# Performance work log

Measured on AMD Instinct MI355X. Metric: run time of the kernel, lower is better.

Reference implementation:

```python
import jax, jax.numpy as jnp
import numpy as np

P, U, D, B = 10000, 8000, 64, 4096
NG, ND, NU, NPU = 320000, 320000, 400000, 400000
TEMP = 0.2
L_GEO, L_DI, L_MV = 2, 2, 2


def _spmm(rows, cols, vals, x, n_out):
    # sparse [n_out, n_in] @ x [n_in, D] as gather + segment-sum (COO spmm)
    return jax.ops.segment_sum(vals[:, None] * x[cols], rows, num_segments=n_out)


def _l2norm(x):
    return x / jnp.maximum(jnp.linalg.norm(x, axis=1, keepdims=True), 1e-12)


def _infonce(e1, e2):
    pos = jnp.exp(jnp.sum(e1 * e2, axis=1) / TEMP)
    neg = jnp.sum(jnp.exp(e1 @ e2.T / TEMP), axis=1)
    return jnp.mean(-jnp.log(pos / (neg + 1e-8) + 1e-8))


def setup_inputs() -> dict:
    key = jax.random.key(0)
    ks = jax.random.split(key, 32)
    f = jax.random.normal
    ri = jax.random.randint
    return {
        "poi_emb": f(ks[0], (P + 1, D)) * 0.1,
        "user_emb": f(ks[1], (U, D)) * 0.1,
        "w_gate_geo": f(ks[2], (D, D)) * 0.1,
        "b_gate_geo": f(ks[3], (1, D)) * 0.1,
        "w_gate_seq": f(ks[4], (D, D)) * 0.1,
        "b_gate_seq": f(ks[5], (1, D)) * 0.1,
        "w_gate_col": f(ks[6], (D, D)) * 0.1,
        "b_gate_col": f(ks[7], (1, D)) * 0.1,
        "fusion_w": f(ks[8], (7 * D, D)) * 0.05,
        "fusion_b": f(ks[9], (D,)) * 0.05,
        "geo_vals": jax.random.uniform(ks[10], (NG,)) / 32.0,
        "src_vals": jax.random.uniform(ks[11], (ND,)) / 32.0,
        "tar_vals": jax.random.uniform(ks[12], (ND,)) / 32.0,
        "up_vals": jax.random.uniform(ks[13], (NU,)) / 50.0,
        "pu_vals": jax.random.uniform(ks[14], (NPU,)) / 50.0,
        "geo_rows": ri(ks[15], (NG,), 0, P),
        "geo_cols": ri(ks[16], (NG,), 0, P),
        "src_rows": ri(ks[17], (ND,), 0, P),
        "src_cols": ri(ks[18], (ND,), 0, P),
        "tar_rows": ri(ks[19], (ND,), 0, P),
        "tar_cols": ri(ks[20], (ND,), 0, P),
        "up_rows": ri(ks[21], (NU,), 0, U),
        "up_cols": ri(ks[22], (NU,), 0, P),
        "pu_rows": ri(ks[23], (NPU,), 0, P),
        "pu_cols": ri(ks[24], (NPU,), 0, U),
        "user_idx": ri(ks[25], (B,), 0, U),
    }


def reference(poi_emb, user_emb, w_gate_geo, b_gate_geo, w_gate_seq, b_gate_seq,
              w_gate_col, b_gate_col, fusion_w, fusion_b,
              geo_vals, src_vals, tar_vals, up_vals, pu_vals,
              geo_rows, geo_cols, src_rows, src_cols, tar_rows, tar_cols,
              up_rows, up_cols, pu_rows, pu_cols, user_idx):
    pe = poi_emb[:-1]  # [P, D], drop padding row
    gate = lambda w, b: pe * jax.nn.sigmoid(pe @ w + b)
    geo_g = gate(w_gate_geo, b_gate_geo)
    seq_g = gate(w_gate_seq, b_gate_seq)
    col_g = gate(w_gate_col, b_gate_col)

    # GeoConvNetwork: residual spmm layers, mean over all layer outputs
    x = geo_g
    acc = [x]
    for _ in range(L_GEO):
        x = _spmm(geo_rows, geo_cols, geo_vals, x, P) + acc[-1]
        acc.append(x)
    geo_pois = sum(acc) / (L_GEO + 1)

    # DirectedHyperConvNetwork: HG_src @ (HG_tar @ x), residual, mean
    x = seq_g
    acc = [x]
    for _ in range(L_DI):
        m = _spmm(tar_rows, tar_cols, tar_vals, x, P)
        x = _spmm(src_rows, src_cols, src_vals, m, P) + acc[-1]
        acc.append(x)
    seq_pois = sum(acc) / (L_DI + 1)

    ng = _l2norm(geo_pois)
    ns = _l2norm(seq_pois)
    loss_cl = 0.5 * (_infonce(ng, ns) + _infonce(ns, ng))

    # MultiSemanticHyperConvNetwork: layer input is always the init embeddings
    acc = [col_g]
    for _ in range(L_MV):
        m_geo = _spmm(up_rows, up_cols, up_vals, ng, U)
        m_seq = _spmm(up_rows, up_cols, up_vals, ns, U)
        m_poi = _spmm(up_rows, up_cols, up_vals, col_g, U)
        msg = jnp.concatenate([m_geo, m_seq, m_poi,
                               m_geo * m_seq, m_geo * m_poi, m_seq * m_poi,
                               m_geo * m_seq * m_poi], axis=1)  # [U, 7D]
        msg_emb = msg @ fusion_w + fusion_b
        hg_users = msg_emb + user_emb + msg_emb * user_emb
        x = _spmm(pu_rows, pu_cols, pu_vals, hg_users, P) + acc[-1]
        acc.append(x)
    hg_pois = sum(acc) / (L_MV + 1)

    fusion_pois = _l2norm(hg_pois) + ng + ns
    users_struct = _spmm(up_rows, up_cols, up_vals, fusion_pois, U)
    batch_users = _l2norm(users_struct[user_idx])
    return batch_users, fusion_pois, loss_cl
```

## Files before the change

kernel.cpp:

```cpp
#include <hip/hip_runtime.h>

#define PN 10000
#define UN 8000
#define BN 4096
#define NGE 320000
#define NDE 320000
#define NUE 400000
#define NPUE 400000
#define SCALE_BF 2.6857914f
#define E0 320000
#define E1 640000
#define E2 960000
#define E3 1360000
#define E4 1760000

#define SCHUNK 4096
#define NC_A 79
#define NC_B 158
#define NC_C 237
#define NC_D 335
#define NCT 433
#define RPB_P 79
#define RPB_U 63
#define MAGIC_P 53093u
#define MAGIC_U 66577u

#define HW_P 32
#define HW_U 40
#define PT_GEO 0
#define PT_TAR 320000
#define PT_SRC 640000
#define PT_UP  960000
#define PT_PU  1280000

#define NSTR 79

typedef __attribute__((ext_vector_type(8))) short short8;
typedef __attribute__((ext_vector_type(4))) float f32x4;
typedef unsigned short u16;
typedef unsigned int u32;

__device__ __forceinline__ u16 f2bf(float x) {
    u32 u = __float_as_uint(x);
    return (u16)((u + 0x7FFFu + ((u >> 16) & 1u)) >> 16);
}

__global__ void gates3_kernel(const float* __restrict__ poi,
                              const float* __restrict__ w0, const float* __restrict__ b0,
                              const float* __restrict__ w1, const float* __restrict__ b1,
                              const float* __restrict__ w2, const float* __restrict__ b2,
                              float* __restrict__ o0, float* __restrict__ o1, float* __restrict__ o2) {
    __shared__ float W[3][64][64];
    __shared__ float Bv[3][64];
    __shared__ float pe[4][64];
    int tid = threadIdx.x;
    for (int t = tid; t < 4096; t += 256) {
        int k = t >> 6, j = t & 63;
        W[0][k][j] = w0[t]; W[1][k][j] = w1[t]; W[2][k][j] = w2[t];
    }
    if (tid < 64) { Bv[0][tid] = b0[tid]; Bv[1][tid] = b1[tid]; Bv[2][tid] = b2[tid]; }
    int r0 = blockIdx.x * 4;
    {
        int r = tid >> 6, k = tid & 63;
        pe[r][k] = poi[(r0 + r) * 64 + k];
    }
    __syncthreads();
    int r = tid >> 6, j = tid & 63;
    float pj = pe[r][j];
    int o = (r0 + r) * 64 + j;
    float out[3];
#pragma unroll
    for (int g = 0; g < 3; g++) {
        float acc = Bv[g][j];
#pragma unroll
        for (int k = 0; k < 64; k++) acc += pe[r][k] * W[g][k][j];
        out[g] = pj * (1.0f / (1.0f + __expf(-acc)));
    }
    o0[o] = out[0]; o1[o] = out[1]; o2[o] = out[2];
}

__global__ __launch_bounds__(256) void hist_lds_kernel(
        const int* __restrict__ r0, const int* __restrict__ r1,
        const int* __restrict__ r2, const int* __restrict__ r3,
        const int* __restrict__ r4, int* __restrict__ part) {
    __shared__ int h[PN];
    int b = blockIdx.x, tid = threadIdx.x;
    const int* rows; int n; int l; int* pp;
    if (b < 32)       { rows = r0; n = PN; l = b;       pp = part + PT_GEO + l * PN; }
    else if (b < 64)  { rows = r1; n = PN; l = b - 32;  pp = part + PT_TAR + l * PN; }
    else if (b < 96)  { rows = r2; n = PN; l = b - 64;  pp = part + PT_SRC + l * PN; }
    else if (b < 136) { rows = r3; n = UN; l = b - 96;  pp = part + PT_UP  + l * UN; }
    else              { rows = r4; n = PN; l = b - 136; pp = part + PT_PU  + l * PN; }
    for (int i = tid; i < n; i += 256) h[i] = 0;
    __syncthreads();
    int base4 = l * 2500;
    for (int j = tid; j < 2500; j += 256) {
        int4 rv = ((const int4*)rows)[base4 + j];
        atomicAdd(&h[rv.x], 1);
        atomicAdd(&h[rv.y], 1);
        atomicAdd(&h[rv.z], 1);
        atomicAdd(&h[rv.w], 1);
    }
    __syncthreads();
    for (int i = tid; i < n; i += 256) pp[i] = h[i];
}

__global__ __launch_bounds__(256) void sum_partials_kernel(const int* __restrict__ part,
                                                           int* __restrict__ t0, int* __restrict__ t1,
                                                           int* __restrict__ t2, int* __restrict__ t3,
                                                           int* __restrict__ t4) {
    int t = blockIdx.x * 256 + threadIdx.x;
    const int* pp; int* tot; int n; int W; int i;
    if (t < 10000)      { pp = part + PT_GEO; tot = t0; n = PN; W = HW_P; i = t; }
    else if (t < 20000) { pp = part + PT_TAR; tot = t1; n = PN; W = HW_P; i = t - 10000; }
    else if (t < 30000) { pp = part + PT_SRC; tot = t2; n = PN; W = HW_P; i = t - 20000; }
    else if (t < 38000) { pp = part + PT_UP;  tot = t3; n = UN; W = HW_U; i = t - 30000; }
    else if (t < 48000) { pp = part + PT_PU;  tot = t4; n = PN; W = HW_U; i = t - 38000; }
    else return;
    int s = 0;
    for (int w = 0; w < W; w++) s += pp[w * n + i];
    tot[i] = s;
}

__global__ __launch_bounds__(1024) void scan_lds_kernel(
        const int* __restrict__ t0, const int* __restrict__ t1,
        const int* __restrict__ t2, const int* __restrict__ t3,
        const int* __restrict__ t4,
        int* p0, int* p1, int* p2, int* p3, int* p4) {
    __shared__ int h[PN];
    __shared__ int ps[1024];
    const int* tot; int* rp; int n; int nnz;
    switch (blockIdx.x) {
        case 0: tot = t0; rp = p0; n = PN; nnz = NGE;  break;
        case 1: tot = t1; rp = p1; n = PN; nnz = NDE;  break;
        case 2: tot = t2; rp = p2; n = PN; nnz = NDE;  break;
        case 3: tot = t3; rp = p3; n = UN; nnz = NUE;  break;
        default: tot = t4; rp = p4; n = PN; nnz = NPUE; break;
    }
    int tid = threadIdx.x;
    for (int i = tid; i < n; i += 1024) h[i] = tot[i];
    __syncthreads();
    int chunk = (n + 1023) >> 10;
    int base = tid * chunk;
    int s = 0;
#pragma unroll
    for (int k = 0; k < 10; k++) {
        int i = base + k;
        if (k < chunk && i < n) s += h[i];
    }
    ps[tid] = s;
    __syncthreads();
    for (int off = 1; off < 1024; off <<= 1) {
        int v = (tid >= off) ? ps[tid - off] : 0;
        __syncthreads();
        ps[tid] += v;
        __syncthreads();
    }
    int pre = (tid > 0) ? ps[tid - 1] : 0;
#pragma unroll
    for (int k = 0; k < 10; k++) {
        int i = base + k;
        if (k < chunk && i < n) {
            int c = h[i];
            rp[i] = pre;
            pre += c;
        }
    }
    if (tid == 0) rp[n] = nnz;
}

__global__ void init_bcur_kernel(const int* __restrict__ rp0, const int* __restrict__ rp1,
                                 const int* __restrict__ rp2, const int* __restrict__ rp3,
                                 const int* __restrict__ rp4, int* __restrict__ bcur) {
    int t = blockIdx.x * 256 + threadIdx.x;
    if (t >= 640) return;
    int m = t >> 7, b = t & 127;
    const int* rp; int n; int rpb;
    switch (m) {
        case 0: rp = rp0; n = PN; rpb = RPB_P; break;
        case 1: rp = rp1; n = PN; rpb = RPB_P; break;
        case 2: rp = rp2; n = PN; rpb = RPB_P; break;
        case 3: rp = rp3; n = UN; rpb = RPB_U; break;
        default: rp = rp4; n = PN; rpb = RPB_P; break;
    }
    int r = b * rpb; if (r > n) r = n;
    bcur[t] = rp[r];
}

__global__ __launch_bounds__(256) void scatter_p1_kernel(
        const int* __restrict__ r0, const int* __restrict__ k0, const float* __restrict__ v0, int2* __restrict__ t0,
        const int* __restrict__ r1, const int* __restrict__ k1, const float* __restrict__ v1, int2* __restrict__ t1,
        const int* __restrict__ r2, const int* __restrict__ k2, const float* __restrict__ v2, int2* __restrict__ t2,
        const int* __restrict__ r3, const int* __restrict__ k3, const float* __restrict__ v3, int2* __restrict__ t3,
        const int* __restrict__ r4, const int* __restrict__ k4, const float* __restrict__ v4, int2* __restrict__ t4,
        int* __restrict__ bcur) {
    __shared__ int cnt[128];
    __shared__ int2 stage[128 * 64];
    int tid = threadIdx.x;
    int c = blockIdx.x;
    const int* rr; const int* cc; const float* vv; int2* tt; int n; int lc; int m; u32 magic;
    if (c < NC_A)      { rr = r0; cc = k0; vv = v0; tt = t0; n = NGE;  lc = c;        m = 0; magic = MAGIC_P; }
    else if (c < NC_B) { rr = r1; cc = k1; vv = v1; tt = t1; n = NDE;  lc = c - NC_A; m = 1; magic = MAGIC_P; }
    else if (c < NC_C) { rr = r2; cc = k2; vv = v2; tt = t2; n = NDE;  lc = c - NC_B; m = 2; magic = MAGIC_P; }
    else if (c < NC_D) { rr = r3; cc = k3; vv = v3; tt = t3; n = NUE;  lc = c - NC_C; m = 3; magic = MAGIC_U; }
    else               { rr = r4; cc = k4; vv = v4; tt = t4; n = NPUE; lc = c - NC_D; m = 4; magic = MAGIC_P; }
    if (tid < 128) cnt[tid] = 0;
    __syncthreads();
    int* gc = bcur + (m << 7);
    int base4 = lc * (SCHUNK / 4);
#pragma unroll
    for (int s = 0; s < 4; s++) {
        int e4i = base4 + s * 256 + tid;
        if (e4i * 4 < n) {
            int4   rv = ((const int4*)rr)[e4i];
            int4   cv = ((const int4*)cc)[e4i];
            float4 wv = ((const float4*)vv)[e4i];
            int rws[4] = {rv.x, rv.y, rv.z, rv.w};
            int cls[4] = {cv.x, cv.y, cv.z, cv.w};
            float vls[4] = {wv.x, wv.y, wv.z, wv.w};
#pragma unroll
            for (int q = 0; q < 4; q++) {
                int row = rws[q];
                int b = (int)(((u32)row * magic) >> 22);
                int2 ent = make_int2((row << 16) | cls[q], __float_as_int(vls[q]));
                int sl = atomicAdd(&cnt[b], 1);
                if (sl < 64) stage[(b << 6) + sl] = ent;
                else { int p = atomicAdd(&gc[b], 1); tt[p] = ent; }
            }
        }
    }
    __syncthreads();
    if (tid < 128) {
        int cc2 = cnt[tid]; if (cc2 > 64) cc2 = 64;
        if (cc2 > 0) {
            int p = atomicAdd(&gc[tid], cc2);
            for (int k = 0; k < cc2; k++) tt[p + k] = stage[(tid << 6) + k];
        }
    }
}

__global__ __launch_bounds__(256) void scatter_p2_kernel(
        const int* __restrict__ rp0, const int2* __restrict__ t0, int2* __restrict__ e0,
        const int* __restrict__ rp1, const int2* __restrict__ t1, int2* __restrict__ e1,
        const int* __restrict__ rp2, const int2* __restrict__ t2, int2* __restrict__ e2,
        const int* __restrict__ rp3, const int2* __restrict__ t3, int2* __restrict__ e3,
        const int* __restrict__ rp4, const int2* __restrict__ t4, int2* __restrict__ e4) {
    __shared__ int lcur[RPB_P];
    int blk = blockIdx.x;
    int m = blk >> 7, b = blk & 127;
    const int* rp; const int2* tp; int2* en; int nrows; int rpb;
    switch (m) {
        case 0: rp = rp0; tp = t0; en = e0; nrows = PN; rpb = RPB_P; break;
        case 1: rp = rp1; tp = t1; en = e1; nrows = PN; rpb = RPB_P; break;
        case 2: rp = rp2; tp = t2; en = e2; nrows = PN; rpb = RPB_P; break;
        case 3: rp = rp3; tp = t3; en = e3; nrows = UN; rpb = RPB_U; break;
        default: rp = rp4; tp = t4; en = e4; nrows = PN; rpb = RPB_P; break;
    }
    int r0 = b * rpb;
    if (r0 >= nrows) return;
    int r1 = r0 + rpb; if (r1 > nrows) r1 = nrows;
    int nr = r1 - r0;
    int tid = threadIdx.x;
    if (tid < nr) lcur[tid] = rp[r0 + tid];
    __syncthreads();
    int s = rp[r0], e = rp[r1];
    for (int k = s + tid; k < e; k += 256) {
        int2 t = tp[k];
        int row = (int)(((u32)t.x) >> 16);
        int col = t.x & 0xFFFF;
        int p = atomicAdd(&lcur[row - r0], 1);
        en[p] = make_int2(col, t.y);
    }
}

struct SpmmJob {
    const int* rp; const int2* ent; const float* x; const float* add;
    const float* avg_a; const float* avg_b; float* y; u16* yb;
    int nrows; int mode;
};

__global__ void spmm_jobs_kernel(SpmmJob ja, SpmmJob jb, int nb0) {
    bool first = ((int)blockIdx.x < nb0);
    SpmmJob J; int blk;
    if (first) { J = ja; blk = blockIdx.x; }
    else       { J = jb; blk = blockIdx.x - nb0; }
    int lane = threadIdx.x & 63;
    int row = blk * 4 + (threadIdx.x >> 6);
    if (row >= J.nrows) return;
    size_t o = (size_t)row * 64 + lane;
    int s = J.rp[row], e = J.rp[row + 1];
    float acc = J.add ? J.add[o] : 0.0f;
    int p = s;
    for (; p + 8 <= e; p += 8) {
        int2 c0 = J.ent[p], c1 = J.ent[p + 1], c2 = J.ent[p + 2], c3 = J.ent[p + 3];
        int2 c4 = J.ent[p + 4], c5 = J.ent[p + 5], c6 = J.ent[p + 6], c7 = J.ent[p + 7];
        float w0 = J.x[(size_t)c0.x * 64 + lane];
        float w1 = J.x[(size_t)c1.x * 64 + lane];
        float w2 = J.x[(size_t)c2.x * 64 + lane];
        float w3 = J.x[(size_t)c3.x * 64 + lane];
        float w4 = J.x[(size_t)c4.x * 64 + lane];
        float w5 = J.x[(size_t)c5.x * 64 + lane];
        float w6 = J.x[(size_t)c6.x * 64 + lane];
        float w7 = J.x[(size_t)c7.x * 64 + lane];
        acc = fmaf(__int_as_float(c0.y), w0, acc);
        acc = fmaf(__int_as_float(c1.y), w1, acc);
        acc = fmaf(__int_as_float(c2.y), w2, acc);
        acc = fmaf(__int_as_float(c3.y), w3, acc);
        acc = fmaf(__int_as_float(c4.y), w4, acc);
        acc = fmaf(__int_as_float(c5.y), w5, acc);
        acc = fmaf(__int_as_float(c6.y), w6, acc);
        acc = fmaf(__int_as_float(c7.y), w7, acc);
    }
    for (; p + 4 <= e; p += 4) {
        int2 c0 = J.ent[p], c1 = J.ent[p + 1], c2 = J.ent[p + 2], c3 = J.ent[p + 3];
        float w0 = J.x[(size_t)c0.x * 64 + lane];
        float w1 = J.x[(size_t)c1.x * 64 + lane];
        float w2 = J.x[(size_t)c2.x * 64 + lane];
        float w3 = J.x[(size_t)c3.x * 64 + lane];
        acc = fmaf(__int_as_float(c0.y), w0, acc);
        acc = fmaf(__int_as_float(c1.y), w1, acc);
        acc = fmaf(__int_as_float(c2.y), w2, acc);
        acc = fmaf(__int_as_float(c3.y), w3, acc);
    }
    for (; p < e; ++p) {
        int2 c = J.ent[p];
        acc = fmaf(__int_as_float(c.y), J.x[(size_t)c.x * 64 + lane], acc);
    }
    if (J.mode == 0) { J.y[o] = acc; return; }
    float v = (J.avg_a[o] + J.avg_b[o] + acc) * (1.0f / 3.0f);
    float ss = v * v;
#pragma unroll
    for (int off = 32; off > 0; off >>= 1) ss += __shfl_xor(ss, off, 64);
    float d = fmaxf(sqrtf(ss), 1e-12f);
    float r = v / d;
    J.y[o] = r;
    J.yb[o] = f2bf(r * SCALE_BF);
}

__global__ void fuse_users_kernel(const float* __restrict__ a0p, const float* __restrict__ a1p,
                                  const float* __restrict__ a2p, const float* __restrict__ fw,
                                  const float* __restrict__ fb, const float* __restrict__ ue,
                                  float* __restrict__ hg) {
    __shared__ float msg[4][448];
    int tid = threadIdx.x, lane = tid & 63, r = tid >> 6;
    int row = blockIdx.x * 4 + r;
    size_t o = (size_t)row * 64 + lane;
    float a0 = a0p[o], a1 = a1p[o], a2 = a2p[o];
    msg[r][0 * 64 + lane] = a0;
    msg[r][1 * 64 + lane] = a1;
    msg[r][2 * 64 + lane] = a2;
    msg[r][3 * 64 + lane] = a0 * a1;
    msg[r][4 * 64 + lane] = a0 * a2;
    msg[r][5 * 64 + lane] = a1 * a2;
    msg[r][6 * 64 + lane] = a0 * a1 * a2;
    __syncthreads();
    float acc = fb[lane];
#pragma unroll 8
    for (int k = 0; k < 448; k++) acc = fmaf(msg[r][k], fw[k * 64 + lane], acc);
    float u = ue[o];
    hg[o] = acc + u + acc * u;
}

__global__ void pu_out_kernel(const int* __restrict__ rp, const int2* __restrict__ ent,
                              const float* __restrict__ hg, const float* __restrict__ colg,
                              const float* __restrict__ ng, const float* __restrict__ ns,
                              float* __restrict__ fuse, float* __restrict__ outp) {
    int lane = threadIdx.x & 63;
    int row = blockIdx.x * 4 + (threadIdx.x >> 6);
    size_t o = (size_t)row * 64 + lane;
    float acc = colg[o];
    int s = rp[row], e = rp[row + 1];
    int p = s;
    for (; p + 8 <= e; p += 8) {
        int2 c0 = ent[p], c1 = ent[p + 1], c2 = ent[p + 2], c3 = ent[p + 3];
        int2 c4 = ent[p + 4], c5 = ent[p + 5], c6 = ent[p + 6], c7 = ent[p + 7];
        float w0 = hg[(size_t)c0.x * 64 + lane];
        float w1 = hg[(size_t)c1.x * 64 + lane];
        float w2 = hg[(size_t)c2.x * 64 + lane];
        float w3 = hg[(size_t)c3.x * 64 + lane];
        float w4 = hg[(size_t)c4.x * 64 + lane];
        float w5 = hg[(size_t)c5.x * 64 + lane];
        float w6 = hg[(size_t)c6.x * 64 + lane];
        float w7 = hg[(size_t)c7.x * 64 + lane];
        acc = fmaf(__int_as_float(c0.y), w0, acc);
        acc = fmaf(__int_as_float(c1.y), w1, acc);
        acc = fmaf(__int_as_float(c2.y), w2, acc);
        acc = fmaf(__int_as_float(c3.y), w3, acc);
        acc = fmaf(__int_as_float(c4.y), w4, acc);
        acc = fmaf(__int_as_float(c5.y), w5, acc);
        acc = fmaf(__int_as_float(c6.y), w6, acc);
        acc = fmaf(__int_as_float(c7.y), w7, acc);
    }
    for (; p + 4 <= e; p += 4) {
        int2 c0 = ent[p], c1 = ent[p + 1], c2 = ent[p + 2], c3 = ent[p + 3];
        float w0 = hg[(size_t)c0.x * 64 + lane];
        float w1 = hg[(size_t)c1.x * 64 + lane];
        float w2 = hg[(size_t)c2.x * 64 + lane];
        float w3 = hg[(size_t)c3.x * 64 + lane];
        acc = fmaf(__int_as_float(c0.y), w0, acc);
        acc = fmaf(__int_as_float(c1.y), w1, acc);
        acc = fmaf(__int_as_float(c2.y), w2, acc);
        acc = fmaf(__int_as_float(c3.y), w3, acc);
    }
    for (; p < e; ++p) {
        int2 c = ent[p];
        acc = fmaf(__int_as_float(c.y), hg[(size_t)c.x * 64 + lane], acc);
    }
    float ss = acc * acc;
#pragma unroll
    for (int off = 32; off > 0; off >>= 1) ss += __shfl_xor(ss, off, 64);
    float d = fmaxf(sqrtf(ss), 1e-12f);
    float f = acc / d + ng[o] + ns[o];
    fuse[o] = f;
    outp[o] = f;
}

__global__ __launch_bounds__(256) void infonce_mfma_kernel(
        const u16* __restrict__ Ab, const u16* __restrict__ Bb,
        float* __restrict__ rowpart, float* __restrict__ colpart, float* __restrict__ pos) {
    __shared__ __align__(16) char smraw[36864];
    __shared__ float colred[4][64];
    u16* Al = (u16*)smraw;
    u16* Bl = (u16*)(smraw + 18432);
    float* red = (float*)smraw;
    int tid = threadIdx.x;
    int i0 = blockIdx.x * 128, j0 = blockIdx.y * 128;
    const uint4 zero4 = make_uint4(0, 0, 0, 0);
    for (int u = tid; u < 1024; u += 256) {
        int row = u >> 3, ch = u & 7;
        int ga = i0 + row, gb = j0 + row;
        uint4 va = (ga < PN) ? ((const uint4*)Ab)[(size_t)ga * 8 + ch] : zero4;
        uint4 vb = (gb < PN) ? ((const uint4*)Bb)[(size_t)gb * 8 + ch] : zero4;
        ((uint4*)Al)[row * 9 + ch] = va;
        ((uint4*)Bl)[row * 9 + ch] = vb;
    }
    __syncthreads();
    int wv = tid >> 6, lane = tid & 63;
    int wr = (wv & 1) * 64;
    int wc = (wv >> 1) * 64;
    int quad = lane >> 4, l15 = lane & 15;

    short8 af[4][2], bf[4][2];
#pragma unroll
    for (int t = 0; t < 4; t++)
#pragma unroll
        for (int ks = 0; ks < 2; ks++) {
            af[t][ks] = *(const short8*)&Al[(wr + t * 16 + l15) * 72 + ks * 32 + quad * 8];
            bf[t][ks] = *(const short8*)&Bl[(wc + t * 16 + l15) * 72 + ks * 32 + quad * 8];
        }
    __syncthreads();

    f32x4 acc[4][4];
#pragma unroll
    for (int rt = 0; rt < 4; rt++)
#pragma unroll
        for (int ct = 0; ct < 4; ct++) {
            f32x4 c = {0.f, 0.f, 0.f, 0.f};
            c = __builtin_amdgcn_mfma_f32_16x16x32_bf16(af[rt][0], bf[ct][0], c, 0, 0, 0);
            c = __builtin_amdgcn_mfma_f32_16x16x32_bf16(af[rt][1], bf[ct][1], c, 0, 0, 0);
            acc[rt][ct] = c;
        }

    float rs[4][4];
#pragma unroll
    for (int rt = 0; rt < 4; rt++)
#pragma unroll
        for (int g = 0; g < 4; g++) rs[rt][g] = 0.f;
    float cs[4] = {0.f, 0.f, 0.f, 0.f};

    bool interior = (i0 + 128 <= PN) && (j0 + 128 <= PN) && (i0 != j0);
    if (interior) {
#pragma unroll
        for (int rt = 0; rt < 4; rt++)
#pragma unroll
            for (int ct = 0; ct < 4; ct++) {
                float csum = 0.f;
#pragma unroll
                for (int g = 0; g < 4; g++) {
                    float e = __builtin_amdgcn_exp2f(acc[rt][ct][g]);
                    rs[rt][g] += e;
                    csum += e;
                }
                cs[ct] += csum;
            }
    } else {
#pragma unroll
        for (int rt = 0; rt < 4; rt++) {
            int ibase = i0 + wr + rt * 16 + quad * 4;
#pragma unroll
            for (int ct = 0; ct < 4; ct++) {
                int j = j0 + wc + ct * 16 + l15;
                bool jv = (j < PN);
                float csum = 0.f;
#pragma unroll
                for (int g = 0; g < 4; g++) {
                    int i = ibase + g;
                    float e = 0.f;
                    if (jv && i < PN) {
                        e = __builtin_amdgcn_exp2f(acc[rt][ct][g]);
                        if (i == j) pos[i] = e;
                    }
                    rs[rt][g] += e;
                    csum += e;
                }
                cs[ct] += csum;
            }
        }
    }
#pragma unroll
    for (int off = 16; off <= 32; off <<= 1)
#pragma unroll
        for (int ct = 0; ct < 4; ct++) cs[ct] += __shfl_xor(cs[ct], off, 64);
    if (quad == 0) {
#pragma unroll
        for (int ct = 0; ct < 4; ct++) colred[wv][ct * 16 + l15] = cs[ct];
    }
    int slot = (wv >> 1) * 16 + l15;
#pragma unroll
    for (int rt = 0; rt < 4; rt++)
#pragma unroll
        for (int g = 0; g < 4; g++) {
            int rl = wr + rt * 16 + quad * 4 + g;
            red[slot * 131 + rl] = rs[rt][g];
        }
    __syncthreads();
    if (tid < 128) {
        float sum = 0.f;
#pragma unroll
        for (int s2 = 0; s2 < 32; s2++) sum += red[s2 * 131 + tid];
        int i = i0 + tid;
        if (i < PN) rowpart[(size_t)blockIdx.y * PN + i] = sum;
        int half = tid >> 6, jl = tid & 63;
        float cv = colred[half * 2 + 0][jl] + colred[half * 2 + 1][jl];
        int j = j0 + half * 64 + jl;
        if (j < PN) colpart[(size_t)blockIdx.x * PN + j] = cv;
    }
}

__global__ __launch_bounds__(256) void reduce_sums_kernel(
        const float* __restrict__ rowpart, const float* __restrict__ colpart,
        float* __restrict__ rowsum, float* __restrict__ colsum) {
    int t = blockIdx.x * 256 + threadIdx.x;
    if (t >= 2 * PN) return;
    const float* src; float* dst; int i;
    if (t < PN) { src = rowpart; dst = rowsum; i = t; }
    else        { src = colpart; dst = colsum; i = t - PN; }
    float s = 0.f;
    for (int w = 0; w < NSTR; w++) s += src[(size_t)w * PN + i];
    dst[i] = s;
}

__global__ void batch_loss_kernel(const float* __restrict__ us, const int* __restrict__ idx,
                                  float* __restrict__ outb, const float* __restrict__ pos,
                                  const float* __restrict__ n1, const float* __restrict__ n2,
                                  float* __restrict__ outl) {
    __shared__ float red[256];
    int tid = threadIdx.x;
    if ((int)blockIdx.x < 1024) {
        int lane = tid & 63;
        int b = blockIdx.x * 4 + (tid >> 6);
        int r = idx[b];
        float v = us[(size_t)r * 64 + lane];
        float s = v * v;
#pragma unroll
        for (int off = 32; off > 0; off >>= 1) s += __shfl_xor(s, off, 64);
        float d = fmaxf(sqrtf(s), 1e-12f);
        outb[(size_t)b * 64 + lane] = v / d;
        return;
    }
    float acc = 0.0f;
    for (int i = tid; i < PN; i += 256) {
        float p = pos[i];
        acc += -logf(p / (n1[i] + 1e-8f) + 1e-8f);
        acc += -logf(p / (n2[i] + 1e-8f) + 1e-8f);
    }
    red[tid] = acc;
    __syncthreads();
    for (int s = 128; s > 0; s >>= 1) {
        if (tid < s) red[tid] += red[tid + s];
        __syncthreads();
    }
    if (tid == 0) outl[0] = 0.5f * red[0] / (float)PN;
}

extern "C" void kernel_launch(void* const* d_in, const int* in_sizes, int n_in,
                              void* d_out, int out_size, void* d_ws, size_t ws_size,
                              hipStream_t stream) {
    (void)in_sizes; (void)n_in; (void)out_size; (void)ws_size;
    const float* poi  = (const float*)d_in[0];
    const float* uemb = (const float*)d_in[1];
    const float* wgg  = (const float*)d_in[2];
    const float* bgg  = (const float*)d_in[3];
    const float* wgs  = (const float*)d_in[4];
    const float* bgs  = (const float*)d_in[5];
    const float* wgc  = (const float*)d_in[6];
    const float* bgc  = (const float*)d_in[7];
    const float* fw   = (const float*)d_in[8];
    const float* fb   = (const float*)d_in[9];
    const float* geo_vals = (const float*)d_in[10];
    const float* src_vals = (const float*)d_in[11];
    const float* tar_vals = (const float*)d_in[12];
    const float* up_vals  = (const float*)d_in[13];
    const float* pu_vals  = (const float*)d_in[14];
    const int* geo_rows = (const int*)d_in[15];
    const int* geo_cols = (const int*)d_in[16];
    const int* src_rows = (const int*)d_in[17];
    const int* src_cols = (const int*)d_in[18];
    const int* tar_rows = (const int*)d_in[19];
    const int* tar_cols = (const int*)d_in[20];
    const int* up_rows  = (const int*)d_in[21];
    const int* up_cols  = (const int*)d_in[22];
    const int* pu_rows  = (const int*)d_in[23];
    const int* pu_cols  = (const int*)d_in[24];
    const int* user_idx = (const int*)d_in[25];

    const int PD = PN * 64, UD = UN * 64;

    float* F = (float*)d_ws;
    float* rowsum = F;
    float* colsum = rowsum + PN;
    float* pos    = colsum + PN;
    u16*   ngb    = (u16*)(F + 3 * PN);
    u16*   nsb    = ngb + PD;
    float* U0     = F + 3 * PN + PD;
    float* P0     = U0 + UD;
    float* P1     = P0 + PD;
    float* P2     = P1 + PD;
    float* P3     = P2 + PD;
    float* P4     = P3 + PD;
    float* P5     = P4 + PD;

    int* part = (int*)U0;
    int2* tmp = (int2*)U0;
    int2* tmp_geo = tmp;
    int2* tmp_tar = tmp_geo + NGE;
    int2* tmp_src = tmp_tar + NDE;
    int2* tmp_up  = tmp_src + NDE;
    int2* tmp_pu  = tmp_up + NUE;

    int* M = (int*)(P5 + PD);
    int* geo_rp = M;               int* geo_tot = geo_rp + PN + 1;
    int* tar_rp = geo_tot + PN;    int* tar_tot = tar_rp + PN + 1;
    int* src_rp = tar_tot + PN;    int* src_tot = src_rp + PN + 1;
    int* up_rp  = src_tot + PN;    int* up_tot  = up_rp + UN + 1;
    int* pu_rp  = up_tot + UN;     int* pu_tot  = pu_rp + PN + 1;
    int* bcur   = M + 96006;
    const int meta_ints = 96646;
    int2* geo_ent = (int2*)(M + meta_ints);
    int2* tar_ent = geo_ent + NGE;
    int2* src_ent = tar_ent + NDE;
    int2* up_ent  = src_ent + NDE;
    int2* pu_ent  = up_ent + NUE;

    float* rowpart = (float*)geo_ent;
    float* colpart = rowpart + (size_t)NSTR * PN;

    float* out_bu = (float*)d_out;
    float* out_fp = out_bu + (size_t)BN * 64;
    float* out_loss = out_fp + (size_t)PN * 64;

    const int RB = PN / 4;
    const int UB = UN / 4;

    hist_lds_kernel<<<176, 256, 0, stream>>>(geo_rows, tar_rows, src_rows, up_rows, pu_rows, part);
    sum_partials_kernel<<<188, 256, 0, stream>>>(part, geo_tot, tar_tot, src_tot, up_tot, pu_tot);
    scan_lds_kernel<<<5, 1024, 0, stream>>>(geo_tot, tar_tot, src_tot, up_tot, pu_tot,
                                            geo_rp, tar_rp, src_rp, up_rp, pu_rp);
    init_bcur_kernel<<<3, 256, 0, stream>>>(geo_rp, tar_rp, src_rp, up_rp, pu_rp, bcur);
    scatter_p1_kernel<<<NCT, 256, 0, stream>>>(
        geo_rows, geo_cols, geo_vals, tmp_geo,
        tar_rows, tar_cols, tar_vals, tmp_tar,
        src_rows, src_cols, src_vals, tmp_src,
        up_rows, up_cols, up_vals, tmp_up,
        pu_rows, pu_cols, pu_vals, tmp_pu,
        bcur);
    scatter_p2_kernel<<<640, 256, 0, stream>>>(
        geo_rp, tmp_geo, geo_ent,
        tar_rp, tmp_tar, tar_ent,
        src_rp, tmp_src, src_ent,
        up_rp, tmp_up, up_ent,
        pu_rp, tmp_pu, pu_ent);
    gates3_kernel<<<RB, 256, 0, stream>>>(poi, wgg, bgg, wgs, bgs, wgc, bgc, P0, P1, P2);

    SpmmJob jz = {};
    SpmmJob j_geo1 = {geo_rp, geo_ent, P0, P0, nullptr, nullptr, P3, nullptr, PN, 0};
    SpmmJob j_tar1 = {tar_rp, tar_ent, P1, nullptr, nullptr, nullptr, P4, nullptr, PN, 0};
    spmm_jobs_kernel<<<2 * RB, 256, 0, stream>>>(j_geo1, j_tar1, RB);
    SpmmJob j_geo2 = {geo_rp, geo_ent, P3, P3, P0, P3, P0, ngb, PN, 1};
    SpmmJob j_s1   = {src_rp, src_ent, P4, P1, nullptr, nullptr, P5, nullptr, PN, 0};
    spmm_jobs_kernel<<<2 * RB, 256, 0, stream>>>(j_geo2, j_s1, RB);
    SpmmJob j_tar2 = {tar_rp, tar_ent, P5, nullptr, nullptr, nullptr, P4, nullptr, PN, 0};
    spmm_jobs_kernel<<<RB, 256, 0, stream>>>(j_tar2, jz, RB);
    SpmmJob j_s2 = {src_rp, src_ent, P4, P5, P1, P5, P1, nsb, PN, 1};
    spmm_jobs_kernel<<<RB, 256, 0, stream>>>(j_s2, jz, RB);
    dim3 ig(NSTR, NSTR);
    infonce_mfma_kernel<<<ig, 256, 0, stream>>>(ngb, nsb, rowpart, colpart, pos);
    reduce_sums_kernel<<<(2 * PN + 255) / 256, 256, 0, stream>>>(rowpart, colpart, rowsum, colsum);
    SpmmJob j_mg = {up_rp, up_ent, P0, nullptr, nullptr, nullptr, P4, nullptr, UN, 0};
    SpmmJob j_ms = {up_rp, up_ent, P1, nullptr, nullptr, nullptr, P3, nullptr, UN, 0};
    spmm_jobs_kernel<<<2 * UB, 256, 0, stream>>>(j_mg, j_ms, UB);
    SpmmJob j_mp = {up_rp, up_ent, P2, nullptr, nullptr, nullptr, U0, nullptr, UN, 0};
    spmm_jobs_kernel<<<UB, 256, 0, stream>>>(j_mp, jz, UB);
    fuse_users_kernel<<<UB, 256, 0, stream>>>(P4, P3, U0, fw, fb, uemb, U0);
    pu_out_kernel<<<RB, 256, 0, stream>>>(pu_rp, pu_ent, U0, P2, P0, P1, P3, out_fp);
    SpmmJob j_upf = {up_rp, up_ent, P3, nullptr, nullptr, nullptr, U0, nullptr, UN, 0};
    spmm_jobs_kernel<<<UB, 256, 0, stream>>>(j_upf, jz, UB);
    batch_loss_kernel<<<1025, 256, 0, stream>>>(U0, user_idx, out_bu, pos, rowsum, colsum, out_loss);
}
```

Measured before the change: 416.9 us.

## Fuse bcur init into scan, spmm into fuse-users and batch gather

Result: faster. 396.2 us (-5.0%).

```diff
diff --git a/kernel.cpp b/kernel.cpp
--- a/kernel.cpp
+++ b/kernel.cpp
@@ -126,16 +126,16 @@
         const int* __restrict__ t0, const int* __restrict__ t1,
         const int* __restrict__ t2, const int* __restrict__ t3,
         const int* __restrict__ t4,
-        int* p0, int* p1, int* p2, int* p3, int* p4) {
+        int* p0, int* p1, int* p2, int* p3, int* p4, int* __restrict__ bcur) {
     __shared__ int h[PN];
     __shared__ int ps[1024];
-    const int* tot; int* rp; int n; int nnz;
+    const int* tot; int* rp; int n; int nnz; int rpb;
     switch (blockIdx.x) {
-        case 0: tot = t0; rp = p0; n = PN; nnz = NGE;  break;
-        case 1: tot = t1; rp = p1; n = PN; nnz = NDE;  break;
-        case 2: tot = t2; rp = p2; n = PN; nnz = NDE;  break;
-        case 3: tot = t3; rp = p3; n = UN; nnz = NUE;  break;
-        default: tot = t4; rp = p4; n = PN; nnz = NPUE; break;
+        case 0: tot = t0; rp = p0; n = PN; nnz = NGE;  rpb = RPB_P; break;
+        case 1: tot = t1; rp = p1; n = PN; nnz = NDE;  rpb = RPB_P; break;
+        case 2: tot = t2; rp = p2; n = PN; nnz = NDE;  rpb = RPB_P; break;
+        case 3: tot = t3; rp = p3; n = UN; nnz = NUE;  rpb = RPB_U; break;
+        default: tot = t4; rp = p4; n = PN; nnz = NPUE; rpb = RPB_P; break;
     }
     int tid = threadIdx.x;
     for (int i = tid; i < n; i += 1024) h[i] = tot[i];
@@ -163,28 +163,16 @@
         if (k < chunk && i < n) {
             int c = h[i];
             rp[i] = pre;
+            h[i] = pre;
             pre += c;
         }
     }
     if (tid == 0) rp[n] = nnz;
-}
-
-__global__ void init_bcur_kernel(const int* __restrict__ rp0, const int* __restrict__ rp1,
-                                 const int* __restrict__ rp2, const int* __restrict__ rp3,
-                                 const int* __restrict__ rp4, int* __restrict__ bcur) {
-    int t = blockIdx.x * 256 + threadIdx.x;
-    if (t >= 640) return;
-    int m = t >> 7, b = t & 127;
-    const int* rp; int n; int rpb;
-    switch (m) {
-        case 0: rp = rp0; n = PN; rpb = RPB_P; break;
-        case 1: rp = rp1; n = PN; rpb = RPB_P; break;
-        case 2: rp = rp2; n = PN; rpb = RPB_P; break;
-        case 3: rp = rp3; n = UN; rpb = RPB_U; break;
-        default: rp = rp4; n = PN; rpb = RPB_P; break;
-    }
-    int r = b * rpb; if (r > n) r = n;
-    bcur[t] = rp[r];
+    __syncthreads();
+    if (tid < 128) {
+        int r = tid * rpb; if (r > n) r = n;
+        bcur[blockIdx.x * 128 + tid] = (r == n) ? nnz : h[r];
+    }
 }
 
 __global__ __launch_bounds__(256) void scatter_p1_kernel(
@@ -279,6 +267,48 @@
     int nrows; int mode;
 };
 
+__device__ __forceinline__ float spmm_row_acc(const int2* __restrict__ ent,
+                                              const float* __restrict__ x,
+                                              int s, int e, int lane, float acc) {
+    int p = s;
+    for (; p + 8 <= e; p += 8) {
+        int2 c0 = ent[p], c1 = ent[p + 1], c2 = ent[p + 2], c3 = ent[p + 3];
+        int2 c4 = ent[p + 4], c5 = ent[p + 5], c6 = ent[p + 6], c7 = ent[p + 7];
+        float w0 = x[(size_t)c0.x * 64 + lane];
+        float w1 = x[(size_t)c1.x * 64 + lane];
+        float w2 = x[(size_t)c2.x * 64 + lane];
+        float w3 = x[(size_t)c3.x * 64 + lane];
+        float w4 = x[(size_t)c4.x * 64 + lane];
+        float w5 = x[(size_t)c5.x * 64 + lane];
+        float w6 = x[(size_t)c6.x * 64 + lane];
+        float w7 = x[(size_t)c7.x * 64 + lane];
+        acc = fmaf(__int_as_float(c0.y), w0, acc);
+        acc = fmaf(__int_as_float(c1.y), w1, acc);
+        acc = fmaf(__int_as_float(c2.y), w2, acc);
+        acc = fmaf(__int_as_float(c3.y), w3, acc);
+        acc = fmaf(__int_as_float(c4.y), w4, acc);
+        acc = fmaf(__int_as_float(c5.y), w5, acc);
+        acc = fmaf(__int_as_float(c6.y), w6, acc);
+        acc = fmaf(__int_as_float(c7.y), w7, acc);
+    }
+    for (; p + 4 <= e; p += 4) {
+        int2 c0 = ent[p], c1 = ent[p + 1], c2 = ent[p + 2], c3 = ent[p + 3];
+        float w0 = x[(size_t)c0.x * 64 + lane];
+        float w1 = x[(size_t)c1.x * 64 + lane];
+        float w2 = x[(size_t)c2.x * 64 + lane];
+        float w3 = x[(size_t)c3.x * 64 + lane];
+        acc = fmaf(__int_as_float(c0.y), w0, acc);
+        acc = fmaf(__int_as_float(c1.y), w1, acc);
+        acc = fmaf(__int_as_float(c2.y), w2, acc);
+        acc = fmaf(__int_as_float(c3.y), w3, acc);
+    }
+    for (; p < e; ++p) {
+        int2 c = ent[p];
+        acc = fmaf(__int_as_float(c.y), x[(size_t)c.x * 64 + lane], acc);
+    }
+    return acc;
+}
+
 __global__ void spmm_jobs_kernel(SpmmJob ja, SpmmJob jb, int nb0) {
     bool first = ((int)blockIdx.x < nb0);
     SpmmJob J; int blk;
@@ -288,44 +318,8 @@
     int row = blk * 4 + (threadIdx.x >> 6);
     if (row >= J.nrows) return;
     size_t o = (size_t)row * 64 + lane;
-    int s = J.rp[row], e = J.rp[row + 1];
     float acc = J.add ? J.add[o] : 0.0f;
-    int p = s;
-    for (; p + 8 <= e; p += 8) {
-        int2 c0 = J.ent[p], c1 = J.ent[p + 1], c2 = J.ent[p + 2], c3 = J.ent[p + 3];
-        int2 c4 = J.ent[p + 4], c5 = J.ent[p + 5], c6 = J.ent[p + 6], c7 = J.ent[p + 7];
-        float w0 = J.x[(size_t)c0.x * 64 + lane];
-        float w1 = J.x[(size_t)c1.x * 64 + lane];
-        float w2 = J.x[(size_t)c2.x * 64 + lane];
-        float w3 = J.x[(size_t)c3.x * 64 + lane];
-        float w4 = J.x[(size_t)c4.x * 64 + lane];
-        float w5 = J.x[(size_t)c5.x * 64 + lane];
-        float w6 = J.x[(size_t)c6.x * 64 + lane];
-        float w7 = J.x[(size_t)c7.x * 64 + lane];
-        acc = fmaf(__int_as_float(c0.y), w0, acc);
-        acc = fmaf(__int_as_float(c1.y), w1, acc);
-        acc = fmaf(__int_as_float(c2.y), w2, acc);
-        acc = fmaf(__int_as_float(c3.y), w3, acc);
-        acc = fmaf(__int_as_float(c4.y), w4, acc);
-        acc = fmaf(__int_as_float(c5.y), w5, acc);
-        acc = fmaf(__int_as_float(c6.y), w6, acc);
-        acc = fmaf(__int_as_float(c7.y), w7, acc);
-    }
-    for (; p + 4 <= e; p += 4) {
-        int2 c0 = J.ent[p], c1 = J.ent[p + 1], c2 = J.ent[p + 2], c3 = J.ent[p + 3];
-        float w0 = J.x[(size_t)c0.x * 64 + lane];
-        float w1 = J.x[(size_t)c1.x * 64 + lane];
-        float w2 = J.x[(size_t)c2.x * 64 + lane];
-        float w3 = J.x[(size_t)c3.x * 64 + lane];
-        acc = fmaf(__int_as_float(c0.y), w0, acc);
-        acc = fmaf(__int_as_float(c1.y), w1, acc);
-        acc = fmaf(__int_as_float(c2.y), w2, acc);
-        acc = fmaf(__int_as_float(c3.y), w3, acc);
-    }
-    for (; p < e; ++p) {
-        int2 c = J.ent[p];
-        acc = fmaf(__int_as_float(c.y), J.x[(size_t)c.x * 64 + lane], acc);
-    }
+    acc = spmm_row_acc(J.ent, J.x, J.rp[row], J.rp[row + 1], lane, acc);
     if (J.mode == 0) { J.y[o] = acc; return; }
     float v = (J.avg_a[o] + J.avg_b[o] + acc) * (1.0f / 3.0f);
     float ss = v * v;
@@ -337,15 +331,17 @@
     J.yb[o] = f2bf(r * SCALE_BF);
 }
 
-__global__ void fuse_users_kernel(const float* __restrict__ a0p, const float* __restrict__ a1p,
-                                  const float* __restrict__ a2p, const float* __restrict__ fw,
-                                  const float* __restrict__ fb, const float* __restrict__ ue,
-                                  float* __restrict__ hg) {
+__global__ void fuse_users_spmm_kernel(const int* __restrict__ rp, const int2* __restrict__ ent,
+                                       const float* __restrict__ xc,
+                                       const float* __restrict__ mg, const float* __restrict__ ms,
+                                       const float* __restrict__ fw, const float* __restrict__ fb,
+                                       const float* __restrict__ ue, float* __restrict__ hg) {
     __shared__ float msg[4][448];
     int tid = threadIdx.x, lane = tid & 63, r = tid >> 6;
     int row = blockIdx.x * 4 + r;
     size_t o = (size_t)row * 64 + lane;
-    float a0 = a0p[o], a1 = a1p[o], a2 = a2p[o];
+    float a2 = spmm_row_acc(ent, xc, rp[row], rp[row + 1], lane, 0.0f);
+    float a0 = mg[o], a1 = ms[o];
     msg[r][0 * 64 + lane] = a0;
     msg[r][1 * 64 + lane] = a1;
     msg[r][2 * 64 + lane] = a2;
@@ -368,44 +364,7 @@
     int lane = threadIdx.x & 63;
     int row = blockIdx.x * 4 + (threadIdx.x >> 6);
     size_t o = (size_t)row * 64 + lane;
-    float acc = colg[o];
-    int s = rp[row], e = rp[row + 1];
-    int p = s;
-    for (; p + 8 <= e; p += 8) {
-        int2 c0 = ent[p], c1 = ent[p + 1], c2 = ent[p + 2], c3 = ent[p + 3];
-        int2 c4 = ent[p + 4], c5 = ent[p + 5], c6 = ent[p + 6], c7 = ent[p + 7];
-        float w0 = hg[(size_t)c0.x * 64 + lane];
-        float w1 = hg[(size_t)c1.x * 64 + lane];
-        float w2 = hg[(size_t)c2.x * 64 + lane];
-        float w3 = hg[(size_t)c3.x * 64 + lane];
-        float w4 = hg[(size_t)c4.x * 64 + lane];
-        float w5 = hg[(size_t)c5.x * 64 + lane];
-        float w6 = hg[(size_t)c6.x * 64 + lane];
-        float w7 = hg[(size_t)c7.x * 64 + lane];
-        acc = fmaf(__int_as_float(c0.y), w0, acc);
-        acc = fmaf(__int_as_float(c1.y), w1, acc);
-        acc = fmaf(__int_as_float(c2.y), w2, acc);
-        acc = fmaf(__int_as_float(c3.y), w3, acc);
-        acc = fmaf(__int_as_float(c4.y), w4, acc);
-        acc = fmaf(__int_as_float(c5.y), w5, acc);
-        acc = fmaf(__int_as_float(c6.y), w6, acc);
-        acc = fmaf(__int_as_float(c7.y), w7, acc);
-    }
-    for (; p + 4 <= e; p += 4) {
-        int2 c0 = ent[p], c1 = ent[p + 1], c2 = ent[p + 2], c3 = ent[p + 3];
-        float w0 = hg[(size_t)c0.x * 64 + lane];
-        float w1 = hg[(size_t)c1.x * 64 + lane];
-        float w2 = hg[(size_t)c2.x * 64 + lane];
-        float w3 = hg[(size_t)c3.x * 64 + lane];
-        acc = fmaf(__int_as_float(c0.y), w0, acc);
-        acc = fmaf(__int_as_float(c1.y), w1, acc);
-        acc = fmaf(__int_as_float(c2.y), w2, acc);
-        acc = fmaf(__int_as_float(c3.y), w3, acc);
-    }
-    for (; p < e; ++p) {
-        int2 c = ent[p];
-        acc = fmaf(__int_as_float(c.y), hg[(size_t)c.x * 64 + lane], acc);
-    }
+    float acc = spmm_row_acc(ent, hg, rp[row], rp[row + 1], lane, colg[o]);
     float ss = acc * acc;
 #pragma unroll
     for (int off = 32; off > 0; off >>= 1) ss += __shfl_xor(ss, off, 64);
@@ -550,17 +509,18 @@
     dst[i] = s;
 }
 
-__global__ void batch_loss_kernel(const float* __restrict__ us, const int* __restrict__ idx,
-                                  float* __restrict__ outb, const float* __restrict__ pos,
-                                  const float* __restrict__ n1, const float* __restrict__ n2,
-                                  float* __restrict__ outl) {
+__global__ void batch_spmm_loss_kernel(const int* __restrict__ rp, const int2* __restrict__ ent,
+                                       const float* __restrict__ x, const int* __restrict__ idx,
+                                       float* __restrict__ outb, const float* __restrict__ pos,
+                                       const float* __restrict__ n1, const float* __restrict__ n2,
+                                       float* __restrict__ outl) {
     __shared__ float red[256];
     int tid = threadIdx.x;
     if ((int)blockIdx.x < 1024) {
         int lane = tid & 63;
         int b = blockIdx.x * 4 + (tid >> 6);
         int r = idx[b];
-        float v = us[(size_t)r * 64 + lane];
+        float v = spmm_row_acc(ent, x, rp[r], rp[r + 1], lane, 0.0f);
         float s = v * v;
 #pragma unroll
         for (int off = 32; off > 0; off >>= 1) s += __shfl_xor(s, off, 64);
@@ -665,8 +625,7 @@
     hist_lds_kernel<<<176, 256, 0, stream>>>(geo_rows, tar_rows, src_rows, up_rows, pu_rows, part);
     sum_partials_kernel<<<188, 256, 0, stream>>>(part, geo_tot, tar_tot, src_tot, up_tot, pu_tot);
     scan_lds_kernel<<<5, 1024, 0, stream>>>(geo_tot, tar_tot, src_tot, up_tot, pu_tot,
-                                            geo_rp, tar_rp, src_rp, up_rp, pu_rp);
-    init_bcur_kernel<<<3, 256, 0, stream>>>(geo_rp, tar_rp, src_rp, up_rp, pu_rp, bcur);
+                                            geo_rp, tar_rp, src_rp, up_rp, pu_rp, bcur);
     scatter_p1_kernel<<<NCT, 256, 0, stream>>>(
         geo_rows, geo_cols, geo_vals, tmp_geo,
         tar_rows, tar_cols, tar_vals, tmp_tar,
@@ -699,11 +658,8 @@
     SpmmJob j_mg = {up_rp, up_ent, P0, nullptr, nullptr, nullptr, P4, nullptr, UN, 0};
     SpmmJob j_ms = {up_rp, up_ent, P1, nullptr, nullptr, nullptr, P3, nullptr, UN, 0};
     spmm_jobs_kernel<<<2 * UB, 256, 0, stream>>>(j_mg, j_ms, UB);
-    SpmmJob j_mp = {up_rp, up_ent, P2, nullptr, nullptr, nullptr, U0, nullptr, UN, 0};
-    spmm_jobs_kernel<<<UB, 256, 0, stream>>>(j_mp, jz, UB);
-    fuse_users_kernel<<<UB, 256, 0, stream>>>(P4, P3, U0, fw, fb, uemb, U0);
+    fuse_users_spmm_kernel<<<UB, 256, 0, stream>>>(up_rp, up_ent, P2, P4, P3, fw, fb, uemb, U0);
     pu_out_kernel<<<RB, 256, 0, stream>>>(pu_rp, pu_ent, U0, P2, P0, P1, P3, out_fp);
-    SpmmJob j_upf = {up_rp, up_ent, P3, nullptr, nullptr, nullptr, U0, nullptr, UN, 0};
-    spmm_jobs_kernel<<<UB, 256, 0, stream>>>(j_upf, jz, UB);
-    batch_loss_kernel<<<1025, 256, 0, stream>>>(U0, user_idx, out_bu, pos, rowsum, colsum, out_loss);
-}
+    batch_spmm_loss_kernel<<<1025, 256, 0, stream>>>(up_rp, up_ent, P3, user_idx,
+                                                     out_bu, pos, rowsum, colsum, out_loss);
+}
```
